# Kernel tuning notes

Measured on AMD Instinct MI355X. Metric: run time of the kernel, lower is better.

Reference implementation:

```python
import jax, jax.numpy as jnp
import numpy as np

IN_F = 4096
OUT_F = 4096
Q_LEVELS = 16  # 4-bit


def setup_inputs() -> dict:
    key = jax.random.key(0)
    k = jax.random.split(key, 7)
    input = jax.random.normal(k[0], (4, 128, IN_F), dtype=jnp.float32)
    qweight = jax.random.randint(k[1], (OUT_F, IN_F), 0, Q_LEVELS, dtype=jnp.int32)
    scales = jax.random.uniform(k[2], (OUT_F, 1), dtype=jnp.float32)
    zeros = jax.random.uniform(k[3], (OUT_F, 1), dtype=jnp.float32)
    outlier = jax.random.uniform(k[4], (OUT_F, IN_F), dtype=jnp.float32)
    grad_updates = jax.random.normal(k[5], (OUT_F, IN_F), dtype=jnp.float32)
    bias = jax.random.normal(k[6], (OUT_F,), dtype=jnp.float32)
    return {"input": input, "qweight": qweight, "scales": scales,
            "zeros": zeros, "outlier": outlier,
            "grad_updates": grad_updates, "bias": bias}


def reference(input, qweight, scales, zeros, outlier, grad_updates, bias):
    # dequantize: affine per-output-row quantization -> dense weight [out, in]
    weight = (qweight.astype(jnp.float32) - zeros) * scales
    # sparse outlier correction (densified), scaled by learned GradUpdates
    weight = weight + outlier * grad_updates
    # F.linear: y = x @ W^T + b
    return jnp.einsum('bsi,oi->bso', input, weight) + bias
```

## Files before the change

kernel.cpp:

```cpp
#include <hip/hip_runtime.h>
#include <stdint.h>

#define IN_F   4096
#define OUT_F  4096
#define M_TOT  512
#define KT     (IN_F / 32)
#define BN     64
#define BK     64
#define KSPLIT 4
#define KPB    (IN_F / KSPLIT)
#define NITER  (KPB / BK)

typedef unsigned short u16;
typedef __bf16 bf16x8 __attribute__((ext_vector_type(8)));
typedef float  f32x4  __attribute__((ext_vector_type(4)));

__device__ __forceinline__ u16 f2bf(float x) {
    unsigned u = __float_as_uint(x);
    u += 0x7FFFu + ((u >> 16) & 1u);
    return (u16)(u >> 16);
}

__global__ void pack_a_kernel(const float* __restrict__ in, u16* __restrict__ aws) {
    int t    = blockIdx.x * blockDim.x + threadIdx.x;
    int lane = t & 63;
    int kt   = (t >> 6) & (KT - 1);
    int mt   = t >> 13;
    int m = mt * 16 + (lane & 15);
    int k = kt * 32 + ((lane >> 4) << 3);
    const float* src = in + (size_t)m * IN_F + k;
    float4 a0 = *(const float4*)src;
    float4 a1 = *(const float4*)(src + 4);
    union { u16 u[8]; uint4 v; } pk;
    pk.u[0]=f2bf(a0.x); pk.u[1]=f2bf(a0.y); pk.u[2]=f2bf(a0.z); pk.u[3]=f2bf(a0.w);
    pk.u[4]=f2bf(a1.x); pk.u[5]=f2bf(a1.y); pk.u[6]=f2bf(a1.z); pk.u[7]=f2bf(a1.w);
    *(uint4*)(aws + (size_t)t * 8) = pk.v;
}

__global__ __launch_bounds__(512, 2) void qlinear_kernel(
    const u16*   __restrict__ aws,
    const int*   __restrict__ qw,
    const float* __restrict__ scales,
    const float* __restrict__ zeros,
    const float* __restrict__ outlier,
    const float* __restrict__ grad,
    float*       __restrict__ part)
{
    __shared__ __align__(16) u16 Bsh[2][8 * 64 * 8];

    const int tid  = threadIdx.x;
    const int lane = tid & 63;
    const int wv   = tid >> 6;

    const int nblk = blockIdx.x & 63;
    const int kblk = blockIdx.x >> 6;
    const int n0   = nblk * BN;
    const int k0   = kblk * KPB;

    const int srow = tid >> 3;
    const int schk = tid & 7;
    const int orow = n0 + srow;
    const float sr = scales[orow];
    const float c0 = -zeros[orow] * sr;
    const size_t sgoff = (size_t)orow * IN_F + k0 + schk * 8;
    const int sfrag = ((schk >> 2) << 2) + (srow >> 4);
    const int slane = (srow & 15) | ((schk & 3) << 4);
    u16* sdst0 = &Bsh[0][(sfrag * 64 + slane) * 8];
    u16* sdst1 = &Bsh[1][(sfrag * 64 + slane) * 8];

    const u16* abase = aws + ((size_t)(wv * 4) * KT + (k0 >> 5)) * 512 + lane * 8;

    f32x4 acc[4][4] = {};

    int4 q0r, q1r; float4 o0r, o1r, g0r, g1r;

    auto load_tile = [&](int it) {
        size_t off = sgoff + (size_t)it * BK;
        q0r = *(const int4*)  (qw      + off);
        q1r = *(const int4*)  (qw      + off + 4);
        o0r = *(const float4*)(outlier + off);
        o1r = *(const float4*)(outlier + off + 4);
        g0r = *(const float4*)(grad    + off);
        g1r = *(const float4*)(grad    + off + 4);
    };
    auto store_tile = [&](u16* dst) {
        union { u16 u[8]; uint4 v; } pk;
        pk.u[0] = f2bf(fmaf((float)q0r.x, sr, fmaf(o0r.x, g0r.x, c0)));
        pk.u[1] = f2bf(fmaf((float)q0r.y, sr, fmaf(o0r.y, g0r.y, c0)));
        pk.u[2] = f2bf(fmaf((float)q0r.z, sr, fmaf(o0r.z, g0r.z, c0)));
        pk.u[3] = f2bf(fmaf((float)q0r.w, sr, fmaf(o0r.w, g0r.w, c0)));
        pk.u[4] = f2bf(fmaf((float)q1r.x, sr, fmaf(o1r.x, g1r.x, c0)));
        pk.u[5] = f2bf(fmaf((float)q1r.y, sr, fmaf(o1r.y, g1r.y, c0)));
        pk.u[6] = f2bf(fmaf((float)q1r.z, sr, fmaf(o1r.z, g1r.z, c0)));
        pk.u[7] = f2bf(fmaf((float)q1r.w, sr, fmaf(o1r.w, g1r.w, c0)));
        *(uint4*)dst = pk.v;
    };

    load_tile(0);
    store_tile(sdst0);
    load_tile(1);
    __syncthreads();

    for (int it = 0; it < NITER; ++it) {
        const u16* bbase = &Bsh[it & 1][0];

        bf16x8 af[2][4], bfr[2][4];
        #pragma unroll
        for (int ks = 0; ks < 2; ++ks)
            #pragma unroll
            for (int mf = 0; mf < 4; ++mf)
                af[ks][mf] = *(const bf16x8*)(abase + ((size_t)mf * KT + it * 2 + ks) * 512);
        #pragma unroll
        for (int ks = 0; ks < 2; ++ks)
            #pragma unroll
            for (int nf = 0; nf < 4; ++nf)
                bfr[ks][nf] = *(const bf16x8*)(bbase + ((ks * 4 + nf) * 64 + lane) * 8);

        #pragma unroll
        for (int ks = 0; ks < 2; ++ks)
            #pragma unroll
            for (int mf = 0; mf < 4; ++mf)
                #pragma unroll
                for (int nf = 0; nf < 4; ++nf)
                    acc[mf][nf] = __builtin_amdgcn_mfma_f32_16x16x32_bf16(
                        af[ks][mf], bfr[ks][nf], acc[mf][nf], 0, 0, 0);

        if (it + 1 < NITER) {
            store_tile((it + 1) & 1 ? sdst1 : sdst0);
            if (it + 2 < NITER) load_tile(it + 2);
        }
        __syncthreads();
    }

    float* pout = part + (size_t)kblk * (M_TOT * OUT_F);
    const int cm0 = wv * 64 + ((lane >> 4) << 2);
    const int cn0 = n0 + (lane & 15);
    #pragma unroll
    for (int mf = 0; mf < 4; ++mf)
        #pragma unroll
        for (int nf = 0; nf < 4; ++nf) {
            float* op = pout + (size_t)(cm0 + mf * 16) * OUT_F + cn0 + nf * 16;
            #pragma unroll
            for (int r = 0; r < 4; ++r)
                op[(size_t)r * OUT_F] = acc[mf][nf][r];
        }
}

__global__ void reduce_kernel(const float4* __restrict__ part,
                              const float4* __restrict__ bias,
                              float4* __restrict__ out) {
    int idx = blockIdx.x * blockDim.x + threadIdx.x;
    float4 s = bias[idx & (OUT_F / 4 - 1)];
    const int STRIDE = M_TOT * OUT_F / 4;
    #pragma unroll
    for (int k = 0; k < KSPLIT; ++k) {
        float4 p = part[(size_t)k * STRIDE + idx];
        s.x += p.x; s.y += p.y; s.z += p.z; s.w += p.w;
    }
    out[idx] = s;
}

extern "C" void kernel_launch(void* const* d_in, const int* in_sizes, int n_in,
                              void* d_out, int out_size, void* d_ws, size_t ws_size,
                              hipStream_t stream) {
    const float* input   = (const float*)d_in[0];
    const int*   qweight = (const int*)  d_in[1];
    const float* scales  = (const float*)d_in[2];
    const float* zeros   = (const float*)d_in[3];
    const float* outlier = (const float*)d_in[4];
    const float* grad    = (const float*)d_in[5];
    const float* bias    = (const float*)d_in[6];
    float* out = (float*)d_out;

    u16*   aws  = (u16*)d_ws;
    float* part = (float*)((char*)d_ws + (4u << 20));

    pack_a_kernel<<<(M_TOT * IN_F / 8) / 256, 256, 0, stream>>>(input, aws);
    qlinear_kernel<<<64 * KSPLIT, 512, 0, stream>>>(aws, qweight, scales, zeros,
                                                    outlier, grad, part);
    reduce_kernel<<<(M_TOT * OUT_F / 4) / 256, 256, 0, stream>>>(
        (const float4*)part, (const float4*)bias, (float4*)out);
}
```

Baseline: 233.7 us.

## Warp-specialize qlinear into producer and consumer waves with a 16-deep LDS ring

The GEMM kernel is split into 8 producer waves and 8 consumer waves. Producers dequantize weight tiles into a 16-slot LDS ring, and consumers run MFMA on them, coordinated by shared-memory ready/freed counters instead of block-wide barriers. The N tile shrinks to 32 and the K split drops from 4 to 2, which halves the partial-sum traffic written and read by the reduce kernel. The aim is to hide the weight-streaming and dequantization latency behind the matrix math. In exchange it adds spin-wait overhead, a risk of stalls from the memory ordering, and lower MFMA reuse per B tile.

```diff
diff --git a/kernel.cpp b/kernel.cpp
--- a/kernel.cpp
+++ b/kernel.cpp
@@ -5,11 +5,12 @@
 #define OUT_F  4096
 #define M_TOT  512
 #define KT     (IN_F / 32)
-#define BN     64
+#define BN     32
 #define BK     64
-#define KSPLIT 4
+#define KSPLIT 2
 #define KPB    (IN_F / KSPLIT)
 #define NITER  (KPB / BK)
+#define NBUF   16
 
 typedef unsigned short u16;
 typedef __bf16 bf16x8 __attribute__((ext_vector_type(8)));
@@ -37,7 +38,7 @@
     *(uint4*)(aws + (size_t)t * 8) = pk.v;
 }
 
-__global__ __launch_bounds__(512, 2) void qlinear_kernel(
+__global__ __launch_bounds__(1024, 4) void qlinear_kernel(
     const u16*   __restrict__ aws,
     const int*   __restrict__ qw,
     const float* __restrict__ scales,
@@ -46,104 +47,120 @@
     const float* __restrict__ grad,
     float*       __restrict__ part)
 {
-    __shared__ __align__(16) u16 Bsh[2][8 * 64 * 8];
+    __shared__ __align__(16) u16 Bsh[NBUF][4 * 64 * 8];
+    __shared__ unsigned ready[NBUF];
+    __shared__ unsigned freed[NBUF];
 
     const int tid  = threadIdx.x;
     const int lane = tid & 63;
     const int wv   = tid >> 6;
 
-    const int nblk = blockIdx.x & 63;
-    const int kblk = blockIdx.x >> 6;
-    const int n0   = nblk * BN;
-    const int k0   = kblk * KPB;
-
-    const int srow = tid >> 3;
-    const int schk = tid & 7;
-    const int orow = n0 + srow;
-    const float sr = scales[orow];
-    const float c0 = -zeros[orow] * sr;
-    const size_t sgoff = (size_t)orow * IN_F + k0 + schk * 8;
-    const int sfrag = ((schk >> 2) << 2) + (srow >> 4);
-    const int slane = (srow & 15) | ((schk & 3) << 4);
-    u16* sdst0 = &Bsh[0][(sfrag * 64 + slane) * 8];
-    u16* sdst1 = &Bsh[1][(sfrag * 64 + slane) * 8];
-
-    const u16* abase = aws + ((size_t)(wv * 4) * KT + (k0 >> 5)) * 512 + lane * 8;
-
-    f32x4 acc[4][4] = {};
-
-    int4 q0r, q1r; float4 o0r, o1r, g0r, g1r;
-
-    auto load_tile = [&](int it) {
-        size_t off = sgoff + (size_t)it * BK;
-        q0r = *(const int4*)  (qw      + off);
-        q1r = *(const int4*)  (qw      + off + 4);
-        o0r = *(const float4*)(outlier + off);
-        o1r = *(const float4*)(outlier + off + 4);
-        g0r = *(const float4*)(grad    + off);
-        g1r = *(const float4*)(grad    + off + 4);
-    };
-    auto store_tile = [&](u16* dst) {
-        union { u16 u[8]; uint4 v; } pk;
-        pk.u[0] = f2bf(fmaf((float)q0r.x, sr, fmaf(o0r.x, g0r.x, c0)));
-        pk.u[1] = f2bf(fmaf((float)q0r.y, sr, fmaf(o0r.y, g0r.y, c0)));
-        pk.u[2] = f2bf(fmaf((float)q0r.z, sr, fmaf(o0r.z, g0r.z, c0)));
-        pk.u[3] = f2bf(fmaf((float)q0r.w, sr, fmaf(o0r.w, g0r.w, c0)));
-        pk.u[4] = f2bf(fmaf((float)q1r.x, sr, fmaf(o1r.x, g1r.x, c0)));
-        pk.u[5] = f2bf(fmaf((float)q1r.y, sr, fmaf(o1r.y, g1r.y, c0)));
-        pk.u[6] = f2bf(fmaf((float)q1r.z, sr, fmaf(o1r.z, g1r.z, c0)));
-        pk.u[7] = f2bf(fmaf((float)q1r.w, sr, fmaf(o1r.w, g1r.w, c0)));
-        *(uint4*)dst = pk.v;
-    };
-
-    load_tile(0);
-    store_tile(sdst0);
-    load_tile(1);
+    if (tid < NBUF) { ready[tid] = 0; freed[tid] = 0; }
     __syncthreads();
 
-    for (int it = 0; it < NITER; ++it) {
-        const u16* bbase = &Bsh[it & 1][0];
-
-        bf16x8 af[2][4], bfr[2][4];
+    const int nblk  = blockIdx.x >> 1;
+    const int khalf = blockIdx.x & 1;
+    const int n0    = nblk * BN;
+    const int k0    = khalf * KPB;
+
+    if (wv >= 8) {
+        const int pt   = tid - 512;
+        const int row  = pt >> 4;
+        const int kc4  = (pt & 15) * 4;
+        const int orow = n0 + row;
+        const float sr = scales[orow];
+        const float c0 = -zeros[orow] * sr;
+        const size_t g0 = (size_t)orow * IN_F + k0 + kc4;
+
+        const int j0    = kc4 & 7;
+        const int frag  = ((kc4 >> 5) << 1) + (row >> 4);
+        const int flane = (row & 15) | (((kc4 >> 3) & 3) << 4);
+        const int doff  = (frag * 64 + flane) * 8 + j0;
+
+        int4 qb[2]; float4 ob[2], gb[2];
+        auto ld = [&](int r, int s) {
+            size_t off = g0 + (size_t)r * BK;
+            qb[s] = *(const int4*)  (qw      + off);
+            ob[s] = *(const float4*)(outlier + off);
+            gb[s] = *(const float4*)(grad    + off);
+        };
+        ld(0, 0);
+        ld(1, 1);
+
+        #pragma unroll 2
+        for (int r = 0; r < NITER; ++r) {
+            int b = r & (NBUF - 1);
+            if (r >= NBUF) {
+                unsigned need = 8u * (unsigned)(r / NBUF);
+                while (__hip_atomic_load(&freed[b], __ATOMIC_ACQUIRE,
+                                         __HIP_MEMORY_SCOPE_WORKGROUP) < need)
+                    __builtin_amdgcn_s_sleep(1);
+            }
+            int s = r & 1;
+            union { u16 u[4]; uint2 v; } pk;
+            pk.u[0] = f2bf(fmaf((float)qb[s].x, sr, fmaf(ob[s].x, gb[s].x, c0)));
+            pk.u[1] = f2bf(fmaf((float)qb[s].y, sr, fmaf(ob[s].y, gb[s].y, c0)));
+            pk.u[2] = f2bf(fmaf((float)qb[s].z, sr, fmaf(ob[s].z, gb[s].z, c0)));
+            pk.u[3] = f2bf(fmaf((float)qb[s].w, sr, fmaf(ob[s].w, gb[s].w, c0)));
+            *(uint2*)(&Bsh[b][doff]) = pk.v;
+            if (lane == 0)
+                __hip_atomic_fetch_add(&ready[b], 1u, __ATOMIC_RELEASE,
+                                       __HIP_MEMORY_SCOPE_WORKGROUP);
+            if (r + 2 < NITER) ld(r + 2, s);
+        }
+    } else {
+        const int cw = wv;
+        const u16* abase = aws + ((size_t)(cw * 4) * KT + (size_t)khalf * (KPB / 32)) * 512
+                               + (size_t)lane * 8;
+        f32x4 acc[4][2] = {};
+
+        #pragma unroll 1
+        for (int r = 0; r < NITER; ++r) {
+            int b = r & (NBUF - 1);
+            unsigned need = 8u * (unsigned)(r / NBUF + 1);
+            while (__hip_atomic_load(&ready[b], __ATOMIC_ACQUIRE,
+                                     __HIP_MEMORY_SCOPE_WORKGROUP) < need)
+                __builtin_amdgcn_s_sleep(1);
+
+            const u16* bb = &Bsh[b][0];
+            bf16x8 bfr[2][2], af[2][4];
+            #pragma unroll
+            for (int ks = 0; ks < 2; ++ks)
+                #pragma unroll
+                for (int nf = 0; nf < 2; ++nf)
+                    bfr[ks][nf] = *(const bf16x8*)(bb + ((ks * 2 + nf) * 64 + lane) * 8);
+            #pragma unroll
+            for (int ks = 0; ks < 2; ++ks)
+                #pragma unroll
+                for (int mf = 0; mf < 4; ++mf)
+                    af[ks][mf] = *(const bf16x8*)(abase + ((size_t)mf * KT + r * 2 + ks) * 512);
+            #pragma unroll
+            for (int ks = 0; ks < 2; ++ks)
+                #pragma unroll
+                for (int mf = 0; mf < 4; ++mf)
+                    #pragma unroll
+                    for (int nf = 0; nf < 2; ++nf)
+                        acc[mf][nf] = __builtin_amdgcn_mfma_f32_16x16x32_bf16(
+                            af[ks][mf], bfr[ks][nf], acc[mf][nf], 0, 0, 0);
+
+            if (lane == 0)
+                __hip_atomic_fetch_add(&freed[b], 1u, __ATOMIC_RELEASE,
+                                       __HIP_MEMORY_SCOPE_WORKGROUP);
+        }
+
+        float* pout = part + (size_t)khalf * (M_TOT * OUT_F);
+        const int cm0 = cw * 64 + ((lane >> 4) << 2);
+        const int cn0 = n0 + (lane & 15);
         #pragma unroll
-        for (int ks = 0; ks < 2; ++ks)
-            #pragma unroll
-            for (int mf = 0; mf < 4; ++mf)
-                af[ks][mf] = *(const bf16x8*)(abase + ((size_t)mf * KT + it * 2 + ks) * 512);
-        #pragma unroll
-        for (int ks = 0; ks < 2; ++ks)
-            #pragma unroll
-            for (int nf = 0; nf < 4; ++nf)
-                bfr[ks][nf] = *(const bf16x8*)(bbase + ((ks * 4 + nf) * 64 + lane) * 8);
-
-        #pragma unroll
-        for (int ks = 0; ks < 2; ++ks)
-            #pragma unroll
-            for (int mf = 0; mf < 4; ++mf)
-                #pragma unroll
-                for (int nf = 0; nf < 4; ++nf)
-                    acc[mf][nf] = __builtin_amdgcn_mfma_f32_16x16x32_bf16(
-                        af[ks][mf], bfr[ks][nf], acc[mf][nf], 0, 0, 0);
-
-        if (it + 1 < NITER) {
-            store_tile((it + 1) & 1 ? sdst1 : sdst0);
-            if (it + 2 < NITER) load_tile(it + 2);
-        }
-        __syncthreads();
+        for (int mf = 0; mf < 4; ++mf)
+            #pragma unroll
+            for (int nf = 0; nf < 2; ++nf) {
+                float* op = pout + (size_t)(cm0 + mf * 16) * OUT_F + cn0 + nf * 16;
+                #pragma unroll
+                for (int rr = 0; rr < 4; ++rr)
+                    op[(size_t)rr * OUT_F] = acc[mf][nf][rr];
+            }
     }
-
-    float* pout = part + (size_t)kblk * (M_TOT * OUT_F);
-    const int cm0 = wv * 64 + ((lane >> 4) << 2);
-    const int cn0 = n0 + (lane & 15);
-    #pragma unroll
-    for (int mf = 0; mf < 4; ++mf)
-        #pragma unroll
-        for (int nf = 0; nf < 4; ++nf) {
-            float* op = pout + (size_t)(cm0 + mf * 16) * OUT_F + cn0 + nf * 16;
-            #pragma unroll
-            for (int r = 0; r < 4; ++r)
-                op[(size_t)r * OUT_F] = acc[mf][nf][r];
-        }
 }
 
 __global__ void reduce_kernel(const float4* __restrict__ part,
@@ -176,8 +193,8 @@
     float* part = (float*)((char*)d_ws + (4u << 20));
 
     pack_a_kernel<<<(M_TOT * IN_F / 8) / 256, 256, 0, stream>>>(input, aws);
-    qlinear_kernel<<<64 * KSPLIT, 512, 0, stream>>>(aws, qweight, scales, zeros,
-                                                    outlier, grad, part);
+    qlinear_kernel<<<(OUT_F / BN) * KSPLIT, 1024, 0, stream>>>(
+        aws, qweight, scales, zeros, outlier, grad, part);
     reduce_kernel<<<(M_TOT * OUT_F / 4) / 256, 256, 0, stream>>>(
         (const float4*)part, (const float4*)bias, (float4*)out);
 }
```

Result: slower. 269.7 us (+15.4%).
